# Kernel tuning notes

Hardware: AMD Instinct MI355X
Metric: run time of the kernel (lower is better)

Reference implementation:

```python
import jax, jax.numpy as jnp
import numpy as np

G = 256          # grid side -> V = G*G = 65536 nodes
N_BATCH = 4
DIM = 128
N_LAYERS = 2
BN_EPS = 1e-5


def _grid_edges(g):
    # 4-neighbor grid, directed edges both ways; row-normalized weights 1/deg(row)
    idx = np.arange(g * g).reshape(g, g)
    right = np.stack([idx[:, :-1].ravel(), idx[:, 1:].ravel()], axis=0)
    down = np.stack([idx[:-1, :].ravel(), idx[1:, :].ravel()], axis=0)
    und = np.concatenate([right, down], axis=1)
    rows = np.concatenate([und[0], und[1]])
    cols = np.concatenate([und[1], und[0]])
    deg = np.bincount(rows, minlength=g * g).astype(np.float32)
    w = 1.0 / deg[rows]
    return rows.astype(np.int32), cols.astype(np.int32), w.astype(np.float32)


def setup_inputs() -> dict:
    key = jax.random.key(0)
    k_h, k_ws, k_wn = jax.random.split(key, 3)
    rows, cols, w = _grid_edges(G)
    V = G * G
    scale = 1.0 / np.sqrt(DIM)
    return {
        "H": jax.random.normal(k_h, (N_BATCH, V, DIM), dtype=jnp.float32),
        "edge_rows": jnp.asarray(rows),
        "edge_cols": jnp.asarray(cols),
        "edge_w": jnp.asarray(w),
        "Ws": jax.random.normal(k_ws, (N_LAYERS, DIM, DIM), dtype=jnp.float32) * scale,
        "Wn": jax.random.normal(k_wn, (N_LAYERS, DIM, DIM), dtype=jnp.float32) * scale,
        "gamma": jnp.ones((N_LAYERS, DIM), dtype=jnp.float32),
        "beta": jnp.zeros((N_LAYERS, DIM), dtype=jnp.float32),
    }


def reference(H, edge_rows, edge_cols, edge_w, Ws, Wn, gamma, beta):
    N, V, D = H.shape
    X = H
    for l in range(Ws.shape[0]):
        # sparse A_norm @ X[n] for every n, via gather + weighted scatter-add
        msgs = X[:, edge_cols, :] * edge_w[None, :, None]          # [N, E, D]
        X_nei = jnp.zeros_like(X).at[:, edge_rows, :].add(msgs)    # [N, V, D]
        # w_self(X) + w_nei(X_nei); nn.Linear applies x @ W.T
        Y = jnp.einsum("nvd,ed->nve", X, Ws[l]) + jnp.einsum("nvd,ed->nve", X_nei, Wn[l])
        # BatchNorm1d over flattened (N*V) rows, training-mode batch stats
        Yf = Y.reshape(-1, D)
        mean = jnp.mean(Yf, axis=0)
        var = jnp.mean(jnp.square(Yf - mean), axis=0)  # biased variance
        Yn = (Yf - mean) * jax.lax.rsqrt(var + BN_EPS) * gamma[l] + beta[l]
        X = jax.nn.relu(Yn).reshape(N, V, D)
    return X
```

## Files before the change

### kernel.cpp

```cpp
#include <hip/hip_runtime.h>
#include <stdint.h>

#define GS   256
#define VN   65536
#define DD   128
#define MROWSF 262144.0f
#define EPS  1e-5f

typedef __bf16 bf16x8 __attribute__((ext_vector_type(8)));
typedef float  f32x4  __attribute__((ext_vector_type(4)));

__device__ __forceinline__ unsigned short f2bf(float f) {
    union { __bf16 b; unsigned short u; } v;
    v.b = (__bf16)f;
    return v.u;
}
__device__ __forceinline__ float bf2f(unsigned short u) {
    union { unsigned int u; float f; } v; v.u = ((unsigned int)u) << 16;
    return v.f;
}

__device__ __forceinline__ int sw_u16(int row, int chunk) {
    return row * 256 + (((chunk) ^ (row & 7)) << 3);
}

__global__ __launch_bounds__(256) void prep_w(const float* __restrict__ Ws,
                                              const float* __restrict__ Wn,
                                              unsigned short* __restrict__ Wc) {
    int idx = blockIdx.x * 256 + threadIdx.x;
    int k = idx & 255;
    int n = (idx >> 8) & 127;
    int l = idx >> 15;
    float v = (k < DD) ? Ws[(l * DD + n) * DD + k]
                       : Wn[(l * DD + n) * DD + (k - DD)];
    Wc[idx] = f2bf(v);
}

template<bool APPLY> struct RawV            { using T = float4;  };
template<>           struct RawV<true>      { using T = ushort4; };

template<bool APPLY, bool DSTBF>
__global__ __launch_bounds__(256, 4) void gnn_layer(
    const void* __restrict__ src, const float* __restrict__ affine,
    const unsigned short* __restrict__ Wc, void* __restrict__ dstY,
    float* __restrict__ Pbuf)
{
    using RT = typename RawV<APPLY>::T;
    __shared__ unsigned short A2[64 * 256];
    const int t  = threadIdx.x;
    const int b  = ((blockIdx.x & 7) << 9) | (blockIdx.x >> 3);
    const int nb = b >> 10;
    const int v0 = (b & 1023) << 6;
    const int r  = v0 >> 8;
    const int c0 = v0 & 255;
    const int q  = t & 31;

    float4 sc = make_float4(0.f, 0.f, 0.f, 0.f), sh = sc;
    if (APPLY) {
        sc = reinterpret_cast<const float4*>(affine)[q];
        sh = reinterpret_cast<const float4*>(affine + DD)[q];
    }
    const size_t base_n = (size_t)nb * VN * DD;
    const RT* __restrict__ srcv = reinterpret_cast<const RT*>(src);

    auto cvt = [&](RT u) -> float4 {
        float4 x;
        if (APPLY) {
            const ushort4& s = *reinterpret_cast<const ushort4*>(&u);
            x.x = fmaxf(bf2f(s.x) * sc.x + sh.x, 0.f);
            x.y = fmaxf(bf2f(s.y) * sc.y + sh.y, 0.f);
            x.z = fmaxf(bf2f(s.z) * sc.z + sh.z, 0.f);
            x.w = fmaxf(bf2f(s.w) * sc.w + sh.w, 0.f);
        } else {
            x = *reinterpret_cast<const float4*>(&u);
        }
        return x;
    };
    auto lds_self = [&](int row) -> float4 {
        ushort4 u = *reinterpret_cast<const ushort4*>(&A2[sw_u16(row, q >> 1) + ((q & 1) << 2)]);
        float4 x; x.x = bf2f(u.x); x.y = bf2f(u.y); x.z = bf2f(u.z); x.w = bf2f(u.w);
        return x;
    };

    const int i0 = t >> 5;
    const bool hasu = (r > 0), hasd = (r < GS - 1);
    const float degr = (hasu ? 1.f : 0.f) + (hasd ? 1.f : 0.f);

    RT sraw[8], uraw[8], draw[8];
    #pragma unroll
    for (int it = 0; it < 8; ++it) {
        const int i = i0 + (it << 3);
        const size_t eq = ((base_n + (size_t)(v0 + i) * DD) >> 2) + q;
        sraw[it] = srcv[eq];
        if (hasu) uraw[it] = srcv[eq - (GS * DD / 4)]; else uraw[it] = RT{};
        if (hasd) draw[it] = srcv[eq + (GS * DD / 4)]; else draw[it] = RT{};
    }
    RT lhraw{}, rhraw{};
    const size_t eq00 = ((base_n + (size_t)v0 * DD) >> 2) + q;
    if (i0 == 0 && c0 > 0)       lhraw = srcv[eq00 - (DD / 4)];
    if (i0 == 7 && c0 + 64 < GS) rhraw = srcv[eq00 + 64 * (DD / 4)];

    #pragma unroll
    for (int it = 0; it < 8; ++it) {
        const int i = i0 + (it << 3);
        float4 xs = cvt(sraw[it]);
        ushort4 us;
        us.x = f2bf(xs.x); us.y = f2bf(xs.y); us.z = f2bf(xs.z); us.w = f2bf(xs.w);
        *reinterpret_cast<ushort4*>(&A2[sw_u16(i, q >> 1) + ((q & 1) << 2)]) = us;
    }
    float4 ud[8];
    #pragma unroll
    for (int it = 0; it < 8; ++it) {
        float4 uu = cvt(uraw[it]);
        float4 dd = cvt(draw[it]);
        ud[it] = make_float4(uu.x + dd.x, uu.y + dd.y, uu.z + dd.z, uu.w + dd.w);
    }
    __syncthreads();

    #pragma unroll
    for (int it = 0; it < 8; ++it) {
        const int i = i0 + (it << 3);
        const int c = c0 + i;
        float4 l = make_float4(0.f, 0.f, 0.f, 0.f), rt = l;
        if (i > 0)             l  = lds_self(i - 1);
        else if (c0 > 0)       l  = cvt(lhraw);
        if (i < 63)            rt = lds_self(i + 1);
        else if (c0 + 64 < GS) rt = cvt(rhraw);
        const float degf = degr + (c > 0 ? 1.f : 0.f) + (c < GS - 1 ? 1.f : 0.f);
        const float wd = 1.f / degf;
        ushort4 un;
        un.x = f2bf((ud[it].x + l.x + rt.x) * wd);
        un.y = f2bf((ud[it].y + l.y + rt.y) * wd);
        un.z = f2bf((ud[it].z + l.z + rt.z) * wd);
        un.w = f2bf((ud[it].w + l.w + rt.w) * wd);
        *reinterpret_cast<ushort4*>(&A2[sw_u16(i, 16 + (q >> 1)) + ((q & 1) << 2)]) = un;
    }
    __syncthreads();

    const int lane = t & 63;
    const int wv   = t >> 6;
    const int lr   = lane & 15;
    const int quad = lane >> 4;

    f32x4 acc[4][2];
    const f32x4 zf = {0.f, 0.f, 0.f, 0.f};
    #pragma unroll
    for (int rt2 = 0; rt2 < 4; ++rt2) { acc[rt2][0] = zf; acc[rt2][1] = zf; }

    const unsigned short* wb0 = Wc + (size_t)((wv << 5) + lr) * 256;
    const unsigned short* wb1 = wb0 + 16 * 256;
    #pragma unroll
    for (int s = 0; s < 8; ++s) {
        const int ck = (s << 2) + quad;
        const bf16x8 b0 = *reinterpret_cast<const bf16x8*>(wb0 + (ck << 3));
        const bf16x8 b1 = *reinterpret_cast<const bf16x8*>(wb1 + (ck << 3));
        #pragma unroll
        for (int rt2 = 0; rt2 < 4; ++rt2) {
            const bf16x8 a = *reinterpret_cast<const bf16x8*>(&A2[sw_u16((rt2 << 4) + lr, ck)]);
            acc[rt2][0] = __builtin_amdgcn_mfma_f32_16x16x32_bf16(a, b0, acc[rt2][0], 0, 0, 0);
            acc[rt2][1] = __builtin_amdgcn_mfma_f32_16x16x32_bf16(a, b1, acc[rt2][1], 0, 0, 0);
        }
    }
    __syncthreads();

    float*          dstf = reinterpret_cast<float*>(dstY) + base_n + (size_t)v0 * DD;
    unsigned short* dstb = reinterpret_cast<unsigned short*>(dstY) + base_n + (size_t)v0 * DD;
    float psum[2] = {0.f, 0.f}, psq[2] = {0.f, 0.f};
    #pragma unroll
    for (int ct = 0; ct < 2; ++ct) {
        const int col = (wv << 5) + (ct << 4) + lr;
        #pragma unroll
        for (int rt2 = 0; rt2 < 4; ++rt2) {
            #pragma unroll
            for (int j = 0; j < 4; ++j) {
                const int row = (rt2 << 4) + (quad << 2) + j;
                const float y = acc[rt2][ct][j];
                if (DSTBF) dstb[row * DD + col] = f2bf(y);
                else       dstf[row * DD + col] = y;
                psum[ct] += y; psq[ct] += y * y;
            }
        }
    }
    float* sred = reinterpret_cast<float*>(A2);
    #pragma unroll
    for (int ct = 0; ct < 2; ++ct) {
        float s1 = psum[ct], s2 = psq[ct];
        s1 += __shfl_xor(s1, 16); s2 += __shfl_xor(s2, 16);
        s1 += __shfl_xor(s1, 32); s2 += __shfl_xor(s2, 32);
        if (quad == 0) {
            const int col = (wv << 5) + (ct << 4) + lr;
            sred[col]      = s1;
            sred[DD + col] = s2;
        }
    }
    __syncthreads();
    Pbuf[(size_t)blockIdx.x * 256 + t] = sred[t];
}

__global__ __launch_bounds__(256) void stats_reduce(const float* __restrict__ P,
                                                    float* __restrict__ P2) {
    const int t = threadIdx.x;
    const float* p = P + (size_t)blockIdx.x * 128 * 256 + t;
    float acc = 0.f;
    #pragma unroll 8
    for (int i = 0; i < 128; ++i) acc += p[(size_t)i * 256];
    P2[(size_t)blockIdx.x * 256 + t] = acc;
}

__global__ void finalize_stats(const float* __restrict__ P2,
                               const float* __restrict__ gamma,
                               const float* __restrict__ beta,
                               float* __restrict__ affine) {
    int f = threadIdx.x;
    if (f < DD) {
        float s1 = 0.f, s2 = 0.f;
        #pragma unroll 8
        for (int j = 0; j < 32; ++j) {
            s1 += P2[j * 256 + f];
            s2 += P2[j * 256 + DD + f];
        }
        const float inv = 1.0f / MROWSF;
        float mean  = s1 * inv;
        float var   = s2 * inv - mean * mean;
        float scale = rsqrtf(var + EPS) * gamma[f];
        affine[f]      = scale;
        affine[DD + f] = beta[f] - mean * scale;
    }
}

template<bool SRCBF>
__global__ __launch_bounds__(256) void final_apply(const void* __restrict__ srcY,
                                                   float* __restrict__ out,
                                                   const float* __restrict__ affine) {
    const int t = threadIdx.x;
    const int q = t & 31;
    const float4 sc = reinterpret_cast<const float4*>(affine)[q];
    const float4 sh = reinterpret_cast<const float4*>(affine + DD)[q];
    const size_t idx0 = (size_t)blockIdx.x * 256 + t;
    float4 y[4];
    if (SRCBF) {
        ushort4 u[4];
        #pragma unroll
        for (int it = 0; it < 4; ++it)
            u[it] = reinterpret_cast<const ushort4*>(srcY)[idx0 + (size_t)it * 2097152];
        #pragma unroll
        for (int it = 0; it < 4; ++it) {
            y[it].x = bf2f(u[it].x); y[it].y = bf2f(u[it].y);
            y[it].z = bf2f(u[it].z); y[it].w = bf2f(u[it].w);
        }
    } else {
        #pragma unroll
        for (int it = 0; it < 4; ++it)
            y[it] = reinterpret_cast<const float4*>(srcY)[idx0 + (size_t)it * 2097152];
    }
    #pragma unroll
    for (int it = 0; it < 4; ++it) {
        float4 v = y[it];
        v.x = fmaxf(v.x * sc.x + sh.x, 0.f);
        v.y = fmaxf(v.y * sc.y + sh.y, 0.f);
        v.z = fmaxf(v.z * sc.z + sh.z, 0.f);
        v.w = fmaxf(v.w * sc.w + sh.w, 0.f);
        reinterpret_cast<float4*>(out)[idx0 + (size_t)it * 2097152] = v;
    }
}

extern "C" void kernel_launch(void* const* d_in, const int* in_sizes, int n_in,
                              void* d_out, int out_size, void* d_ws, size_t ws_size,
                              hipStream_t stream) {
    const float* H     = (const float*)d_in[0];
    const float* Ws    = (const float*)d_in[4];
    const float* Wn    = (const float*)d_in[5];
    const float* gamma = (const float*)d_in[6];
    const float* beta  = (const float*)d_in[7];
    float* out = (float*)d_out;
    char*  ws  = (char*)d_ws;

    unsigned short* Wc = (unsigned short*)ws;
    float* P2   = (float*)(ws + 131072);
    float* aff0 = (float*)(ws + 163840);
    float* aff1 = (float*)(ws + 164864);
    float* Pbuf = (float*)(ws + 165888);
    unsigned short* Y0 = (unsigned short*)(ws + 4360192);
    unsigned short* Y1 = (unsigned short*)(ws + 71469056);
    const bool y1bf = (ws_size >= 138577920);

    prep_w<<<256, 256, 0, stream>>>(Ws, Wn, Wc);
    gnn_layer<false, true ><<<4096, 256, 0, stream>>>((const void*)H, nullptr, Wc, (void*)Y0, Pbuf);
    stats_reduce<<<32, 256, 0, stream>>>(Pbuf, P2);
    finalize_stats<<<1, 128, 0, stream>>>(P2, gamma, beta, aff0);
    if (y1bf) {
        gnn_layer<true, true ><<<4096, 256, 0, stream>>>((const void*)Y0, aff0, Wc + 32768, (void*)Y1, Pbuf);
        stats_reduce<<<32, 256, 0, stream>>>(Pbuf, P2);
        finalize_stats<<<1, 128, 0, stream>>>(P2, gamma + DD, beta + DD, aff1);
        final_apply<true ><<<8192, 256, 0, stream>>>((const void*)Y1, out, aff1);
    } else {
        gnn_layer<true, false><<<4096, 256, 0, stream>>>((const void*)Y0, aff0, Wc + 32768, (void*)out, Pbuf);
        stats_reduce<<<32, 256, 0, stream>>>(Pbuf, P2);
        finalize_stats<<<1, 128, 0, stream>>>(P2, gamma + DD, beta + DD, aff1);
        final_apply<false><<<8192, 256, 0, stream>>>((const void*)out, out, aff1);
    }
}
```

Baseline: 390.1 us.

## Process each 64-node tile in two 32-row halves to halve LDS and registers

The fused layer kernel now loops over two 32-node halves of its tile. Each half reuses a 32x256 bf16 LDS buffer and smaller register arrays, and the launch bounds are raised to allow 6 or 8 blocks per CU. The per-block stats are written straight to Pbuf from the wave shuffles, so the LDS reduction and its final barrier go away. The aim is higher occupancy to hide the memory latency of the neighbor gathers. The cost is extra barriers, serialized load-then-compute phases within a block, and more halo loads at the half boundaries.

```diff
diff --git a/kernel.cpp b/kernel.cpp
--- a/kernel.cpp
+++ b/kernel.cpp
@@ -40,13 +40,13 @@
 template<>           struct RawV<true>      { using T = ushort4; };
 
 template<bool APPLY, bool DSTBF>
-__global__ __launch_bounds__(256, 4) void gnn_layer(
+__global__ __launch_bounds__(256, APPLY ? 8 : 6) void gnn_layer(
     const void* __restrict__ src, const float* __restrict__ affine,
     const unsigned short* __restrict__ Wc, void* __restrict__ dstY,
     float* __restrict__ Pbuf)
 {
     using RT = typename RawV<APPLY>::T;
-    __shared__ unsigned short A2[64 * 256];
+    __shared__ unsigned short A2[32 * 256];
     const int t  = threadIdx.x;
     const int b  = ((blockIdx.x & 7) << 9) | (blockIdx.x >> 3);
     const int nb = b >> 10;
@@ -68,7 +68,7 @@
         if (APPLY) {
             const ushort4& s = *reinterpret_cast<const ushort4*>(&u);
             x.x = fmaxf(bf2f(s.x) * sc.x + sh.x, 0.f);
-            x.y = fmaxf(bf2f(s.y) * sc.y + sh.y, 0.f);
+        x.y = fmaxf(bf2f(s.y) * sc.y + sh.y, 0.f);
             x.z = fmaxf(bf2f(s.z) * sc.z + sh.z, 0.f);
             x.w = fmaxf(bf2f(s.w) * sc.w + sh.w, 0.f);
         } else {
@@ -85,103 +85,110 @@
     const int i0 = t >> 5;
     const bool hasu = (r > 0), hasd = (r < GS - 1);
     const float degr = (hasu ? 1.f : 0.f) + (hasd ? 1.f : 0.f);
-
-    RT sraw[8], uraw[8], draw[8];
-    #pragma unroll
-    for (int it = 0; it < 8; ++it) {
-        const int i = i0 + (it << 3);
-        const size_t eq = ((base_n + (size_t)(v0 + i) * DD) >> 2) + q;
-        sraw[it] = srcv[eq];
-        if (hasu) uraw[it] = srcv[eq - (GS * DD / 4)]; else uraw[it] = RT{};
-        if (hasd) draw[it] = srcv[eq + (GS * DD / 4)]; else draw[it] = RT{};
-    }
-    RT lhraw{}, rhraw{};
-    const size_t eq00 = ((base_n + (size_t)v0 * DD) >> 2) + q;
-    if (i0 == 0 && c0 > 0)       lhraw = srcv[eq00 - (DD / 4)];
-    if (i0 == 7 && c0 + 64 < GS) rhraw = srcv[eq00 + 64 * (DD / 4)];
-
-    #pragma unroll
-    for (int it = 0; it < 8; ++it) {
-        const int i = i0 + (it << 3);
-        float4 xs = cvt(sraw[it]);
-        ushort4 us;
-        us.x = f2bf(xs.x); us.y = f2bf(xs.y); us.z = f2bf(xs.z); us.w = f2bf(xs.w);
-        *reinterpret_cast<ushort4*>(&A2[sw_u16(i, q >> 1) + ((q & 1) << 2)]) = us;
-    }
-    float4 ud[8];
-    #pragma unroll
-    for (int it = 0; it < 8; ++it) {
-        float4 uu = cvt(uraw[it]);
-        float4 dd = cvt(draw[it]);
-        ud[it] = make_float4(uu.x + dd.x, uu.y + dd.y, uu.z + dd.z, uu.w + dd.w);
-    }
-    __syncthreads();
-
-    #pragma unroll
-    for (int it = 0; it < 8; ++it) {
-        const int i = i0 + (it << 3);
-        const int c = c0 + i;
-        float4 l = make_float4(0.f, 0.f, 0.f, 0.f), rt = l;
-        if (i > 0)             l  = lds_self(i - 1);
-        else if (c0 > 0)       l  = cvt(lhraw);
-        if (i < 63)            rt = lds_self(i + 1);
-        else if (c0 + 64 < GS) rt = cvt(rhraw);
-        const float degf = degr + (c > 0 ? 1.f : 0.f) + (c < GS - 1 ? 1.f : 0.f);
-        const float wd = 1.f / degf;
-        ushort4 un;
-        un.x = f2bf((ud[it].x + l.x + rt.x) * wd);
-        un.y = f2bf((ud[it].y + l.y + rt.y) * wd);
-        un.z = f2bf((ud[it].z + l.z + rt.z) * wd);
-        un.w = f2bf((ud[it].w + l.w + rt.w) * wd);
-        *reinterpret_cast<ushort4*>(&A2[sw_u16(i, 16 + (q >> 1)) + ((q & 1) << 2)]) = un;
-    }
-    __syncthreads();
+    const float4 z4 = make_float4(0.f, 0.f, 0.f, 0.f);
 
     const int lane = t & 63;
     const int wv   = t >> 6;
     const int lr   = lane & 15;
     const int quad = lane >> 4;
-
-    f32x4 acc[4][2];
-    const f32x4 zf = {0.f, 0.f, 0.f, 0.f};
-    #pragma unroll
-    for (int rt2 = 0; rt2 < 4; ++rt2) { acc[rt2][0] = zf; acc[rt2][1] = zf; }
-
     const unsigned short* wb0 = Wc + (size_t)((wv << 5) + lr) * 256;
     const unsigned short* wb1 = wb0 + 16 * 256;
+
+    float psum[2] = {0.f, 0.f}, psq[2] = {0.f, 0.f};
+
     #pragma unroll
-    for (int s = 0; s < 8; ++s) {
-        const int ck = (s << 2) + quad;
-        const bf16x8 b0 = *reinterpret_cast<const bf16x8*>(wb0 + (ck << 3));
-        const bf16x8 b1 = *reinterpret_cast<const bf16x8*>(wb1 + (ck << 3));
-        #pragma unroll
-        for (int rt2 = 0; rt2 < 4; ++rt2) {
-            const bf16x8 a = *reinterpret_cast<const bf16x8*>(&A2[sw_u16((rt2 << 4) + lr, ck)]);
-            acc[rt2][0] = __builtin_amdgcn_mfma_f32_16x16x32_bf16(a, b0, acc[rt2][0], 0, 0, 0);
-            acc[rt2][1] = __builtin_amdgcn_mfma_f32_16x16x32_bf16(a, b1, acc[rt2][1], 0, 0, 0);
-        }
-    }
-    __syncthreads();
-
-    float*          dstf = reinterpret_cast<float*>(dstY) + base_n + (size_t)v0 * DD;
-    unsigned short* dstb = reinterpret_cast<unsigned short*>(dstY) + base_n + (size_t)v0 * DD;
-    float psum[2] = {0.f, 0.f}, psq[2] = {0.f, 0.f};
-    #pragma unroll
-    for (int ct = 0; ct < 2; ++ct) {
-        const int col = (wv << 5) + (ct << 4) + lr;
-        #pragma unroll
-        for (int rt2 = 0; rt2 < 4; ++rt2) {
+    for (int h = 0; h < 2; ++h) {
+        const int vh  = v0 + (h << 5);
+        const int ch0 = c0 + (h << 5);
+
+        RT sraw[4], uraw[4], draw[4];
+        #pragma unroll
+        for (int it = 0; it < 4; ++it) {
+            const int i = i0 + (it << 3);
+            const size_t eq = ((base_n + (size_t)(vh + i) * DD) >> 2) + q;
+            sraw[it] = srcv[eq];
+            if (hasu) uraw[it] = srcv[eq - (GS * DD / 4)]; else uraw[it] = RT{};
+            if (hasd) draw[it] = srcv[eq + (GS * DD / 4)]; else draw[it] = RT{};
+        }
+        RT lhraw{}, rhraw{};
+        const size_t eqh = ((base_n + (size_t)vh * DD) >> 2) + q;
+        if (i0 == 0 && ch0 > 0)       lhraw = srcv[eqh - (DD / 4)];
+        if (i0 == 7 && ch0 + 32 < GS) rhraw = srcv[eqh + 32 * (DD / 4)];
+
+        if (h == 1) __syncthreads();
+
+        #pragma unroll
+        for (int it = 0; it < 4; ++it) {
+            const int i = i0 + (it << 3);
+            float4 xs = cvt(sraw[it]);
+            ushort4 us;
+            us.x = f2bf(xs.x); us.y = f2bf(xs.y); us.z = f2bf(xs.z); us.w = f2bf(xs.w);
+            *reinterpret_cast<ushort4*>(&A2[sw_u16(i, q >> 1) + ((q & 1) << 2)]) = us;
+        }
+        float4 ud[4];
+        #pragma unroll
+        for (int it = 0; it < 4; ++it) {
+            float4 uu = hasu ? cvt(uraw[it]) : z4;
+            float4 dd = hasd ? cvt(draw[it]) : z4;
+            ud[it] = make_float4(uu.x + dd.x, uu.y + dd.y, uu.z + dd.z, uu.w + dd.w);
+        }
+        __syncthreads();
+
+        #pragma unroll
+        for (int it = 0; it < 4; ++it) {
+            const int i = i0 + (it << 3);
+            const int c = ch0 + i;
+            float4 l = z4, rt = z4;
+            if (i > 0)              l  = lds_self(i - 1);
+            else if (ch0 > 0)       l  = cvt(lhraw);
+            if (i < 31)             rt = lds_self(i + 1);
+            else if (ch0 + 32 < GS) rt = cvt(rhraw);
+            const float degf = degr + (c > 0 ? 1.f : 0.f) + (c < GS - 1 ? 1.f : 0.f);
+            const float wd = 1.f / degf;
+            ushort4 un;
+            un.x = f2bf((ud[it].x + l.x + rt.x) * wd);
+            un.y = f2bf((ud[it].y + l.y + rt.y) * wd);
+            un.z = f2bf((ud[it].z + l.z + rt.z) * wd);
+            un.w = f2bf((ud[it].w + l.w + rt.w) * wd);
+            *reinterpret_cast<ushort4*>(&A2[sw_u16(i, 16 + (q >> 1)) + ((q & 1) << 2)]) = un;
+        }
+        __syncthreads();
+
+        f32x4 acc[2][2];
+        const f32x4 zf = {0.f, 0.f, 0.f, 0.f};
+        acc[0][0] = zf; acc[0][1] = zf; acc[1][0] = zf; acc[1][1] = zf;
+        #pragma unroll
+        for (int s = 0; s < 8; ++s) {
+            const int ck = (s << 2) + quad;
+            const bf16x8 b0 = *reinterpret_cast<const bf16x8*>(wb0 + (ck << 3));
+            const bf16x8 b1 = *reinterpret_cast<const bf16x8*>(wb1 + (ck << 3));
             #pragma unroll
-            for (int j = 0; j < 4; ++j) {
-                const int row = (rt2 << 4) + (quad << 2) + j;
-                const float y = acc[rt2][ct][j];
-                if (DSTBF) dstb[row * DD + col] = f2bf(y);
-                else       dstf[row * DD + col] = y;
-                psum[ct] += y; psq[ct] += y * y;
+            for (int rt2 = 0; rt2 < 2; ++rt2) {
+                const bf16x8 a = *reinterpret_cast<const bf16x8*>(&A2[sw_u16((rt2 << 4) + lr, ck)]);
+                acc[rt2][0] = __builtin_amdgcn_mfma_f32_16x16x32_bf16(a, b0, acc[rt2][0], 0, 0, 0);
+                acc[rt2][1] = __builtin_amdgcn_mfma_f32_16x16x32_bf16(a, b1, acc[rt2][1], 0, 0, 0);
             }
         }
-    }
-    float* sred = reinterpret_cast<float*>(A2);
+
+        float*          dstf = reinterpret_cast<float*>(dstY) + base_n + (size_t)vh * DD;
+        unsigned short* dstb = reinterpret_cast<unsigned short*>(dstY) + base_n + (size_t)vh * DD;
+        #pragma unroll
+        for (int ct = 0; ct < 2; ++ct) {
+            const int col = (wv << 5) + (ct << 4) + lr;
+            #pragma unroll
+            for (int rt2 = 0; rt2 < 2; ++rt2) {
+                #pragma unroll
+                for (int j = 0; j < 4; ++j) {
+                    const int row = (rt2 << 4) + (quad << 2) + j;
+                    const float y = acc[rt2][ct][j];
+                    if (DSTBF) dstb[row * DD + col] = f2bf(y);
+                    else       dstf[row * DD + col] = y;
+                    psum[ct] += y; psq[ct] += y * y;
+                }
+            }
+        }
+    }
+
     #pragma unroll
     for (int ct = 0; ct < 2; ++ct) {
         float s1 = psum[ct], s2 = psq[ct];
@@ -189,12 +196,10 @@
         s1 += __shfl_xor(s1, 32); s2 += __shfl_xor(s2, 32);
         if (quad == 0) {
             const int col = (wv << 5) + (ct << 4) + lr;
-            sred[col]      = s1;
-            sred[DD + col] = s2;
-        }
-    }
-    __syncthreads();
-    Pbuf[(size_t)blockIdx.x * 256 + t] = sred[t];
+            Pbuf[(size_t)blockIdx.x * 256 + col]      = s1;
+            Pbuf[(size_t)blockIdx.x * 256 + DD + col] = s2;
+        }
+    }
 }
 
 __global__ __launch_bounds__(256) void stats_reduce(const float* __restrict__ P,
```

After: 666.2 us. +70.8%, slower.
